# Performance work log

Measured on AMD Instinct MI355X. Metric: run time of the kernel, lower is better.

## Reference

```python
import jax, jax.numpy as jnp
import numpy as np

B, S, D, H = 2, 2048, 1024, 16
HD = D // H  # head dim = 64


def setup_inputs() -> dict:
    key = jax.random.key(0)
    ks = jax.random.split(key, 9)
    s = 1.0 / np.sqrt(D)
    return {
        "hidden_states": jax.random.normal(ks[0], (B, S, D), dtype=jnp.float32),
        "attention_mask": jnp.zeros((B, 1, 1, S), dtype=jnp.float32),
        "Wq": jax.random.normal(ks[1], (D, D), dtype=jnp.float32) * s,
        "bq": jnp.zeros((D,), dtype=jnp.float32),
        "Wk": jax.random.normal(ks[2], (D, D), dtype=jnp.float32) * s,
        "bk": jnp.zeros((D,), dtype=jnp.float32),
        "Wv": jax.random.normal(ks[3], (D, D), dtype=jnp.float32) * s,
        "bv": jnp.zeros((D,), dtype=jnp.float32),
        "Wo": jax.random.normal(ks[4], (D, D), dtype=jnp.float32) * s,
        "bo": jnp.zeros((D,), dtype=jnp.float32),
    }


def reference(hidden_states, attention_mask, Wq, bq, Wk, bk, Wv, bv, Wo, bo):
    b, s = hidden_states.shape[:2]
    # QKV projections -> [b, h, s, hd]
    def proj(W, bias):
        y = hidden_states @ W.T + bias
        return y.reshape(b, s, H, HD).transpose(0, 2, 1, 3)
    q = proj(Wq, bq)
    k = proj(Wk, bk)
    v = proj(Wv, bv)
    scores = jnp.einsum("bhqd,bhkd->bhqk", q, k) / jnp.sqrt(jnp.float32(HD))
    scores = scores + attention_mask  # additive mask, broadcast [b,1,1,s]
    probs = jax.nn.softmax(scores, axis=-1)  # dropout p=0 (eval)
    ctx = jnp.einsum("bhqk,bhkd->bhqd", probs, v)
    ctx = ctx.transpose(0, 2, 1, 3).reshape(b, s, D)
    out = ctx @ Wo.T + bo
    return (out, probs)
```

## Files before the change

kernel.cpp:

```cpp
#include <hip/hip_runtime.h>
#include <hip/hip_bf16.h>

#define B_ 2
#define S_ 2048
#define D_ 1024
#define H_ 16
#define HD_ 64

typedef short bf16x8 __attribute__((ext_vector_type(8)));
typedef float f32x4 __attribute__((ext_vector_type(4)));

typedef __attribute__((address_space(3))) void lds_void;
typedef const __attribute__((address_space(1))) void gbl_void;

__device__ __forceinline__ f32x4 mfma16(bf16x8 a, bf16x8 b, f32x4 c) {
    return __builtin_amdgcn_mfma_f32_16x16x32_bf16(a, b, c, 0, 0, 0);
}

__device__ __forceinline__ bf16x8 ldb8(const __hip_bfloat16* p) {
    return *reinterpret_cast<const bf16x8*>(p);
}

__global__ __launch_bounds__(256) void conv_kernel(const float* __restrict__ src,
                                                   __hip_bfloat16* __restrict__ dst, int n4) {
    int i = blockIdx.x * 256 + threadIdx.x;
    if (i >= n4) return;
    float4 f = reinterpret_cast<const float4*>(src)[i];
    union { __hip_bfloat16 h[4]; ushort4 u; } cv;
    cv.h[0] = __float2bfloat16(f.x);
    cv.h[1] = __float2bfloat16(f.y);
    cv.h[2] = __float2bfloat16(f.z);
    cv.h[3] = __float2bfloat16(f.w);
    reinterpret_cast<ushort4*>(dst)[i] = cv.u;
}

template <int MODE>
__global__ __launch_bounds__(256) void gemm_bt(
    const __hip_bfloat16* __restrict__ X, const __hip_bfloat16* __restrict__ Wt,
    const float* __restrict__ bias0, const float* __restrict__ bias1,
    const float* __restrict__ bias2,
    __hip_bfloat16* __restrict__ Yq, __hip_bfloat16* __restrict__ Yk,
    __hip_bfloat16* __restrict__ Yv, float* __restrict__ Yo,
    int M, int N, int K) {
    __shared__ __hip_bfloat16 As[128 * 32];
    __shared__ __hip_bfloat16 Bs[128 * 32];

    const int ntn = N >> 7;
    const int nwg = (M >> 7) * ntn;
    const int cpx = nwg >> 3;
    const int bid = blockIdx.x;
    const int lg = (bid & 7) * cpx + (bid >> 3);
    const int tm = lg / ntn;
    const int tn = lg % ntn;
    const int t = threadIdx.x;
    const int w = t >> 6, l = t & 63, g = l >> 4, c = l & 15;
    const int wr = w >> 1, wc = w & 1;

    const int lrow16 = l >> 2;
    const int lcol = (l & 3) * 8;

    const int r0 = w * 32 + lrow16;
    const int r1 = w * 32 + 16 + lrow16;
    const size_t xg0 = (size_t)(tm * 128 + r0) * K + lcol;
    const size_t xg1 = (size_t)(tm * 128 + r1) * K + lcol;
    const size_t wg0 = (size_t)(tn * 128 + r0) * K + lcol;
    const size_t wg1 = (size_t)(tn * 128 + r1) * K + lcol;

    f32x4 acc[4][4] = {};

    for (int k0 = 0; k0 < K; k0 += 32) {
        __syncthreads();
        __builtin_amdgcn_global_load_lds((gbl_void*)(X + xg0 + k0),
                                         (lds_void*)(As + (w * 32) * 32), 16, 0, 0);
        __builtin_amdgcn_global_load_lds((gbl_void*)(X + xg1 + k0),
                                         (lds_void*)(As + (w * 32 + 16) * 32), 16, 0, 0);
        __builtin_amdgcn_global_load_lds((gbl_void*)(Wt + wg0 + k0),
                                         (lds_void*)(Bs + (w * 32) * 32), 16, 0, 0);
        __builtin_amdgcn_global_load_lds((gbl_void*)(Wt + wg1 + k0),
                                         (lds_void*)(Bs + (w * 32 + 16) * 32), 16, 0, 0);
        __syncthreads();

        bf16x8 am[4], bn[4];
#pragma unroll
        for (int mi = 0; mi < 4; ++mi) am[mi] = ldb8(&As[(wr * 64 + mi * 16 + c) * 32 + g * 8]);
#pragma unroll
        for (int ni = 0; ni < 4; ++ni) bn[ni] = ldb8(&Bs[(wc * 64 + ni * 16 + c) * 32 + g * 8]);
#pragma unroll
        for (int mi = 0; mi < 4; ++mi)
#pragma unroll
            for (int ni = 0; ni < 4; ++ni)
                acc[mi][ni] = mfma16(am[mi], bn[ni], acc[mi][ni]);
    }

#pragma unroll
    for (int mi = 0; mi < 4; ++mi) {
        const int mbase = tm * 128 + wr * 64 + mi * 16 + g * 4;
#pragma unroll
        for (int ni = 0; ni < 4; ++ni) {
            const int n = tn * 128 + wc * 64 + ni * 16 + c;
#pragma unroll
            for (int r = 0; r < 4; ++r) {
                const int mm = mbase + r;
                float v = acc[mi][ni][r];
                if (MODE == 0) {
                    const float* bp = (n < 1024) ? bias0 : (n < 2048) ? bias1 : bias2;
                    const int nn = n & 1023;
                    v += bp[nn];
                    const int b = mm >> 11, s = mm & 2047;
                    const int h = nn >> 6, hd = nn & 63;
                    const size_t bh = (size_t)(b * H_ + h);
                    const __hip_bfloat16 bvv = __float2bfloat16(v);
                    if (n < 2048) {
                        __hip_bfloat16* dst = (n < 1024) ? Yq : Yk;
                        dst[(bh * S_ + s) * HD_ + hd] = bvv;
                    } else {
                        Yv[(bh * HD_ + hd) * S_ + s] = bvv;
                    }
                } else {
                    Yo[(size_t)mm * N + n] = v + bias0[n];
                }
            }
        }
    }
}

#define STAGE_K(dstc, t8v) do {                                                   \
    const int kt_ = (t8v) * 256;                                                  \
    _Pragma("unroll")                                                             \
    for (int i_ = 0; i_ < 4; ++i_) {                                              \
        const int chunk_ = w * 4 + i_;                                            \
        const int row_ = 8 * chunk_ + (l >> 3);                                   \
        const int col_ = ((l & 7) ^ ((l >> 3) & 7)) * 8;                          \
        __builtin_amdgcn_global_load_lds(                                         \
            (gbl_void*)(Kb + (size_t)(kt_ + row_) * HD_ + col_),                  \
            (lds_void*)((dstc) + chunk_ * 1024), 16, 0, 0);                       \
    }                                                                             \
} while (0)

#define STAGE_V(dstc, t8v) do {                                                   \
    const int kt_ = (t8v) * 256;                                                  \
    _Pragma("unroll")                                                             \
    for (int i_ = 0; i_ < 4; ++i_) {                                              \
        const int chunk_ = w * 4 + i_;                                            \
        const int row_ = 2 * chunk_ + (l >> 5);                                   \
        const int col_ = ((l & 31) ^ (row_ & 7)) * 8;                             \
        __builtin_amdgcn_global_load_lds(                                         \
            (gbl_void*)(Vb + (size_t)row_ * S_ + kt_ + col_),                     \
            (lds_void*)((dstc) + chunk_ * 1024), 16, 0, 0);                       \
    }                                                                             \
} while (0)

__global__ __launch_bounds__(512) void attn_kernel(
    const __hip_bfloat16* __restrict__ Qh, const __hip_bfloat16* __restrict__ Kh,
    const __hip_bfloat16* __restrict__ Vt, const float* __restrict__ mask,
    float* __restrict__ probs, __hip_bfloat16* __restrict__ ctx) {
    union SMem {
        char Kdb[2][32768];
        float Cred[8][16][68];
    };
    __shared__ SMem sm;
    __shared__ float msk[2048];
    __shared__ float sred[8][32];
    __shared__ float invsh[32];

    const int bid = blockIdx.x;
    const int lg = (bid & 7) * 256 + (bid >> 3);
    const int qt = lg & 63;
    const int bh = lg >> 6;
    const int b = bh >> 4, h = bh & 15;
    const int t = threadIdx.x;
    const int w = t >> 6, l = t & 63, g = l >> 4, c = l & 15;
    const int q0 = qt * 32;
    const int kw = 32 * w;

    const __hip_bfloat16* Qb = Qh + (size_t)bh * S_ * HD_;
    const __hip_bfloat16* Kb = Kh + (size_t)bh * S_ * HD_;
    const __hip_bfloat16* Vb = Vt + (size_t)bh * HD_ * S_;
    const float* mrow = mask + (size_t)b * S_;

    *reinterpret_cast<float4*>(&msk[t * 4]) =
        *reinterpret_cast<const float4*>(&mrow[t * 4]);

    const bf16x8 aqA0 = ldb8(&Qb[(q0 + c) * HD_ + g * 8]);
    const bf16x8 aqA1 = ldb8(&Qb[(q0 + c) * HD_ + 32 + g * 8]);
    const bf16x8 aqB0 = ldb8(&Qb[(q0 + 16 + c) * HD_ + g * 8]);
    const bf16x8 aqB1 = ldb8(&Qb[(q0 + 16 + c) * HD_ + 32 + g * 8]);

    unsigned int uA[8][2][2], uB[8][2][2];
    float lsumA = 0.f, lsumB = 0.f;

    STAGE_K(sm.Kdb[0], 0);
#pragma unroll
    for (int t8 = 0; t8 < 8; ++t8) {
        char* cur = sm.Kdb[t8 & 1];
        if (t8 < 7) {
            STAGE_K(sm.Kdb[(t8 & 1) ^ 1], t8 + 1);
            asm volatile("s_waitcnt vmcnt(4)" ::: "memory");
        } else {
            asm volatile("s_waitcnt vmcnt(0)" ::: "memory");
        }
        if (t8 == 0) asm volatile("s_waitcnt lgkmcnt(0)" ::: "memory");
        __builtin_amdgcn_s_barrier();
        __builtin_amdgcn_sched_barrier(0);
        const int kt = t8 * 256;
#pragma unroll
        for (int ss = 0; ss < 2; ++ss) {
            const int krow = kw + ss * 16 + c;
            const char* kb2 = cur + krow * 128;
            const int sw = (krow & 7) << 4;
            const bf16x8 k0 = *reinterpret_cast<const bf16x8*>(kb2 + ((g * 16) ^ sw));
            const bf16x8 k1 = *reinterpret_cast<const bf16x8*>(kb2 + ((64 + g * 16) ^ sw));
            f32x4 aA = {}, aB = {};
            aA = mfma16(k0, aqA0, aA);
            aA = mfma16(k1, aqA1, aA);
            aB = mfma16(k0, aqB0, aB);
            aB = mfma16(k1, aqB1, aB);
            const float4 mk = *reinterpret_cast<const float4*>(&msk[kt + kw + ss * 16 + g * 4]);
            const float pA0 = __expf(aA[0] * 0.125f + mk.x);
            const float pA1 = __expf(aA[1] * 0.125f + mk.y);
            const float pA2 = __expf(aA[2] * 0.125f + mk.z);
            const float pA3 = __expf(aA[3] * 0.125f + mk.w);
            const float pB0 = __expf(aB[0] * 0.125f + mk.x);
            const float pB1 = __expf(aB[1] * 0.125f + mk.y);
            const float pB2 = __expf(aB[2] * 0.125f + mk.z);
            const float pB3 = __expf(aB[3] * 0.125f + mk.w);
            lsumA += (pA0 + pA1) + (pA2 + pA3);
            lsumB += (pB0 + pB1) + (pB2 + pB3);
            union { __hip_bfloat16 hh[2]; unsigned int ui; } w0, w1;
            w0.hh[0] = __float2bfloat16(pA0); w0.hh[1] = __float2bfloat16(pA1);
            w1.hh[0] = __float2bfloat16(pA2); w1.hh[1] = __float2bfloat16(pA3);
            uA[t8][ss][0] = w0.ui; uA[t8][ss][1] = w1.ui;
            w0.hh[0] = __float2bfloat16(pB0); w0.hh[1] = __float2bfloat16(pB1);
            w1.hh[0] = __float2bfloat16(pB2); w1.hh[1] = __float2bfloat16(pB3);
            uB[t8][ss][0] = w0.ui; uB[t8][ss][1] = w1.ui;
        }
        __builtin_amdgcn_sched_barrier(0);
        __builtin_amdgcn_s_barrier();
    }
    lsumA += __shfl_xor(lsumA, 16); lsumA += __shfl_xor(lsumA, 32);
    lsumB += __shfl_xor(lsumB, 16); lsumB += __shfl_xor(lsumB, 32);
    if (g == 0) { sred[w][c] = lsumA; sred[w][16 + c] = lsumB; }
    __syncthreads();
    float totA = 0.f, totB = 0.f;
#pragma unroll
    for (int w8 = 0; w8 < 8; ++w8) { totA += sred[w8][c]; totB += sred[w8][16 + c]; }
    const float invA = 1.0f / totA;
    const float invB = 1.0f / totB;
    if (w == 0 && g == 0) { invsh[c] = invA; invsh[16 + c] = invB; }

    f32x4 caccA[4] = {}, caccB[4] = {};
    float* prowA = probs + ((size_t)bh * S_ + q0 + c) * S_;
    float* prowB = prowA + (size_t)16 * S_;
    const int src0 = 32 * (g & 1) + c;
    const int src1 = src0 + 16;
    const int sigma = g >> 1;
    STAGE_V(sm.Kdb[0], 0);
#pragma unroll
    for (int t8 = 0; t8 < 8; ++t8) {
        char* cur = sm.Kdb[t8 & 1];
        if (t8 < 7) STAGE_V(sm.Kdb[(t8 & 1) ^ 1], t8 + 1);
        if (t8 == 0 || t8 == 7) asm volatile("s_waitcnt vmcnt(4)" ::: "memory");
        else                    asm volatile("s_waitcnt vmcnt(8)" ::: "memory");
        if (t8 == 0) asm volatile("s_waitcnt lgkmcnt(0)" ::: "memory");
        __builtin_amdgcn_s_barrier();
        __builtin_amdgcn_sched_barrier(0);
        const int kt = t8 * 256;
#pragma unroll
        for (int ss = 0; ss < 2; ++ss) {
            f32x4 oA, oB;
            oA[0] = __uint_as_float(uA[t8][ss][0] << 16) * invA;
            oA[1] = __uint_as_float(uA[t8][ss][0] & 0xffff0000u) * invA;
            oA[2] = __uint_as_float(uA[t8][ss][1] << 16) * invA;
            oA[3] = __uint_as_float(uA[t8][ss][1] & 0xffff0000u) * invA;
            *reinterpret_cast<f32x4*>(&prowA[kt + kw + ss * 16 + g * 4]) = oA;
            oB[0] = __uint_as_float(uB[t8][ss][0] << 16) * invB;
            oB[1] = __uint_as_float(uB[t8][ss][0] & 0xffff0000u) * invB;
            oB[2] = __uint_as_float(uB[t8][ss][1] << 16) * invB;
            oB[3] = __uint_as_float(uB[t8][ss][1] & 0xffff0000u) * invB;
            *reinterpret_cast<f32x4*>(&prowB[kt + kw + ss * 16 + g * 4]) = oB;
        }
        union { unsigned int ui[4]; bf16x8 v; } afA, afB;
        {
            const unsigned int x00 = __shfl(uA[t8][0][0], src0);
            const unsigned int x10 = __shfl(uA[t8][1][0], src0);
            const unsigned int x01 = __shfl(uA[t8][0][1], src0);
            const unsigned int x11 = __shfl(uA[t8][1][1], src0);
            const unsigned int x02 = __shfl(uA[t8][0][0], src1);
            const unsigned int x12 = __shfl(uA[t8][1][0], src1);
            const unsigned int x03 = __shfl(uA[t8][0][1], src1);
            const unsigned int x13 = __shfl(uA[t8][1][1], src1);
            afA.ui[0] = sigma ? x10 : x00;
            afA.ui[1] = sigma ? x11 : x01;
            afA.ui[2] = sigma ? x12 : x02;
            afA.ui[3] = sigma ? x13 : x03;
        }
        {
            const unsigned int x00 = __shfl(uB[t8][0][0], src0);
            const unsigned int x10 = __shfl(uB[t8][1][0], src0);
            const unsigned int x01 = __shfl(uB[t8][0][1], src0);
            const unsigned int x11 = __shfl(uB[t8][1][1], src0);
            const unsigned int x02 = __shfl(uB[t8][0][0], src1);
            const unsigned int x12 = __shfl(uB[t8][1][0], src1);
            const unsigned int x03 = __shfl(uB[t8][0][1], src1);
            const unsigned int x13 = __shfl(uB[t8][1][1], src1);
            afB.ui[0] = sigma ? x10 : x00;
            afB.ui[1] = sigma ? x11 : x01;
            afB.ui[2] = sigma ? x12 : x02;
            afB.ui[3] = sigma ? x13 : x03;
        }
#pragma unroll
        for (int n = 0; n < 4; ++n) {
            const int vrow = n * 16 + c;
            const bf16x8 bv = *reinterpret_cast<const bf16x8*>(
                cur + vrow * 512 + ((64 * w + g * 16) ^ ((vrow & 7) << 4)));
            caccA[n] = mfma16(afA.v, bv, caccA[n]);
            caccB[n] = mfma16(afB.v, bv, caccB[n]);
        }
        __builtin_amdgcn_sched_barrier(0);
        __builtin_amdgcn_s_barrier();
    }

    __syncthreads();
#pragma unroll
    for (int n = 0; n < 4; ++n)
#pragma unroll
        for (int r = 0; r < 4; ++r)
            sm.Cred[w][g * 4 + r][n * 16 + c] = caccA[n][r];
    __syncthreads();
    {
        const int row = t >> 5, col2 = (t & 31) * 2;
        float a0 = 0.f, a1 = 0.f;
#pragma unroll
        for (int w8 = 0; w8 < 8; ++w8) {
            const float2 vv = *reinterpret_cast<const float2*>(&sm.Cred[w8][row][col2]);
            a0 += vv.x; a1 += vv.y;
        }
        const float fin = invsh[row];
        union { __hip_bfloat16 hh[2]; unsigned int ui; } ov;
        ov.hh[0] = __float2bfloat16(a0 * fin);
        ov.hh[1] = __float2bfloat16(a1 * fin);
        *reinterpret_cast<unsigned int*>(
            &ctx[((size_t)b * S_ + q0 + row) * D_ + h * HD_ + col2]) = ov.ui;
    }
    __syncthreads();
#pragma unroll
    for (int n = 0; n < 4; ++n)
#pragma unroll
        for (int r = 0; r < 4; ++r)
            sm.Cred[w][g * 4 + r][n * 16 + c] = caccB[n][r];
    __syncthreads();
    {
        const int row = t >> 5, col2 = (t & 31) * 2;
        float a0 = 0.f, a1 = 0.f;
#pragma unroll
        for (int w8 = 0; w8 < 8; ++w8) {
            const float2 vv = *reinterpret_cast<const float2*>(&sm.Cred[w8][row][col2]);
            a0 += vv.x; a1 += vv.y;
        }
        const float fin = invsh[16 + row];
        union { __hip_bfloat16 hh[2]; unsigned int ui; } ov;
        ov.hh[0] = __float2bfloat16(a0 * fin);
        ov.hh[1] = __float2bfloat16(a1 * fin);
        *reinterpret_cast<unsigned int*>(
            &ctx[((size_t)b * S_ + q0 + 16 + row) * D_ + h * HD_ + col2]) = ov.ui;
    }
}

extern "C" void kernel_launch(void* const* d_in, const int* in_sizes, int n_in,
                              void* d_out, int out_size, void* d_ws, size_t ws_size,
                              hipStream_t stream) {
    const float* hs   = (const float*)d_in[0];
    const float* mask = (const float*)d_in[1];
    const float* Wq   = (const float*)d_in[2];
    const float* bq   = (const float*)d_in[3];
    const float* Wk   = (const float*)d_in[4];
    const float* bk   = (const float*)d_in[5];
    const float* Wv   = (const float*)d_in[6];
    const float* bv   = (const float*)d_in[7];
    const float* Wo   = (const float*)d_in[8];
    const float* bo   = (const float*)d_in[9];

    float* out   = (float*)d_out;
    float* probs = out + (size_t)B_ * S_ * D_;

    const size_t MD = (size_t)B_ * S_ * D_;
    __hip_bfloat16* hsb   = (__hip_bfloat16*)d_ws;
    __hip_bfloat16* wqkvb = hsb + MD;
    __hip_bfloat16* wob   = wqkvb + 3u * 1024u * 1024u;
    __hip_bfloat16* Qh    = wob + (size_t)1024 * 1024;
    __hip_bfloat16* Kh    = Qh + MD;
    __hip_bfloat16* Vt    = Kh + MD;
    __hip_bfloat16* ctxb  = Vt + MD;

    conv_kernel<<<4096, 256, 0, stream>>>(hs, hsb, (int)(MD / 4));
    conv_kernel<<<1024, 256, 0, stream>>>(Wq, wqkvb, 262144);
    conv_kernel<<<1024, 256, 0, stream>>>(Wk, wqkvb + 1048576, 262144);
    conv_kernel<<<1024, 256, 0, stream>>>(Wv, wqkvb + 2097152, 262144);
    conv_kernel<<<1024, 256, 0, stream>>>(Wo, wob, 262144);

    gemm_bt<0><<<32 * 24, 256, 0, stream>>>(hsb, wqkvb, bq, bk, bv,
                                            Qh, Kh, Vt, nullptr, 4096, 3072, 1024);

    attn_kernel<<<B_ * H_ * (S_ / 32), 512, 0, stream>>>(Qh, Kh, Vt, mask, probs, ctxb);

    gemm_bt<1><<<32 * 8, 256, 0, stream>>>(ctxb, wob, bo, nullptr, nullptr,
                                           nullptr, nullptr, nullptr, out, 4096, 1024, 1024);
}
```

Before: 325.8 us.

## Halve attention query tile to 16 rows per block for more parallelism

Each attention block now handles 16 query rows instead of 32. This doubles the grid size and roughly halves per-thread register state: one set of probability accumulators and one context accumulator set instead of two. The launch bounds now request 4 blocks per CU, and the vmcnt waits are adjusted for the smaller number of outstanding stores. The cost is that each K/V tile is reloaded twice as often and fewer MFMAs are amortized per LDS read, while LDS use per block may still cap how many blocks fit on a CU.

```diff
diff --git a/kernel.cpp b/kernel.cpp
--- a/kernel.cpp
+++ b/kernel.cpp
@@ -150,7 +150,7 @@
     }                                                                             \
 } while (0)
 
-__global__ __launch_bounds__(512) void attn_kernel(
+__global__ __launch_bounds__(512, 4) void attn_kernel(
     const __hip_bfloat16* __restrict__ Qh, const __hip_bfloat16* __restrict__ Kh,
     const __hip_bfloat16* __restrict__ Vt, const float* __restrict__ mask,
     float* __restrict__ probs, __hip_bfloat16* __restrict__ ctx) {
@@ -160,17 +160,17 @@
     };
     __shared__ SMem sm;
     __shared__ float msk[2048];
-    __shared__ float sred[8][32];
-    __shared__ float invsh[32];
+    __shared__ float sred[8][16];
+    __shared__ float invsh[16];
 
     const int bid = blockIdx.x;
-    const int lg = (bid & 7) * 256 + (bid >> 3);
-    const int qt = lg & 63;
-    const int bh = lg >> 6;
+    const int lg = (bid & 7) * 512 + (bid >> 3);
+    const int qt = lg & 127;
+    const int bh = lg >> 7;
     const int b = bh >> 4, h = bh & 15;
     const int t = threadIdx.x;
     const int w = t >> 6, l = t & 63, g = l >> 4, c = l & 15;
-    const int q0 = qt * 32;
+    const int q0 = qt * 16;
     const int kw = 32 * w;
 
     const __hip_bfloat16* Qb = Qh + (size_t)bh * S_ * HD_;
@@ -181,13 +181,11 @@
     *reinterpret_cast<float4*>(&msk[t * 4]) =
         *reinterpret_cast<const float4*>(&mrow[t * 4]);
 
-    const bf16x8 aqA0 = ldb8(&Qb[(q0 + c) * HD_ + g * 8]);
-    const bf16x8 aqA1 = ldb8(&Qb[(q0 + c) * HD_ + 32 + g * 8]);
-    const bf16x8 aqB0 = ldb8(&Qb[(q0 + 16 + c) * HD_ + g * 8]);
-    const bf16x8 aqB1 = ldb8(&Qb[(q0 + 16 + c) * HD_ + 32 + g * 8]);
-
-    unsigned int uA[8][2][2], uB[8][2][2];
-    float lsumA = 0.f, lsumB = 0.f;
+    const bf16x8 aq0 = ldb8(&Qb[(q0 + c) * HD_ + g * 8]);
+    const bf16x8 aq1 = ldb8(&Qb[(q0 + c) * HD_ + 32 + g * 8]);
+
+    unsigned int uA[8][2][2];
+    float lsum = 0.f;
 
     STAGE_K(sm.Kdb[0], 0);
 #pragma unroll
@@ -210,76 +208,60 @@
             const int sw = (krow & 7) << 4;
             const bf16x8 k0 = *reinterpret_cast<const bf16x8*>(kb2 + ((g * 16) ^ sw));
             const bf16x8 k1 = *reinterpret_cast<const bf16x8*>(kb2 + ((64 + g * 16) ^ sw));
-            f32x4 aA = {}, aB = {};
-            aA = mfma16(k0, aqA0, aA);
-            aA = mfma16(k1, aqA1, aA);
-            aB = mfma16(k0, aqB0, aB);
-            aB = mfma16(k1, aqB1, aB);
+            f32x4 aA = {};
+            aA = mfma16(k0, aq0, aA);
+            aA = mfma16(k1, aq1, aA);
             const float4 mk = *reinterpret_cast<const float4*>(&msk[kt + kw + ss * 16 + g * 4]);
-            const float pA0 = __expf(aA[0] * 0.125f + mk.x);
-            const float pA1 = __expf(aA[1] * 0.125f + mk.y);
-            const float pA2 = __expf(aA[2] * 0.125f + mk.z);
-            const float pA3 = __expf(aA[3] * 0.125f + mk.w);
-            const float pB0 = __expf(aB[0] * 0.125f + mk.x);
-            const float pB1 = __expf(aB[1] * 0.125f + mk.y);
-            const float pB2 = __expf(aB[2] * 0.125f + mk.z);
-            const float pB3 = __expf(aB[3] * 0.125f + mk.w);
-            lsumA += (pA0 + pA1) + (pA2 + pA3);
-            lsumB += (pB0 + pB1) + (pB2 + pB3);
+            const float p0 = __expf(aA[0] * 0.125f + mk.x);
+            const float p1 = __expf(aA[1] * 0.125f + mk.y);
+            const float p2 = __expf(aA[2] * 0.125f + mk.z);
+            const float p3 = __expf(aA[3] * 0.125f + mk.w);
+            lsum += (p0 + p1) + (p2 + p3);
             union { __hip_bfloat16 hh[2]; unsigned int ui; } w0, w1;
-            w0.hh[0] = __float2bfloat16(pA0); w0.hh[1] = __float2bfloat16(pA1);
-            w1.hh[0] = __float2bfloat16(pA2); w1.hh[1] = __float2bfloat16(pA3);
+            w0.hh[0] = __float2bfloat16(p0); w0.hh[1] = __float2bfloat16(p1);
+            w1.hh[0] = __float2bfloat16(p2); w1.hh[1] = __float2bfloat16(p3);
             uA[t8][ss][0] = w0.ui; uA[t8][ss][1] = w1.ui;
-            w0.hh[0] = __float2bfloat16(pB0); w0.hh[1] = __float2bfloat16(pB1);
-            w1.hh[0] = __float2bfloat16(pB2); w1.hh[1] = __float2bfloat16(pB3);
-            uB[t8][ss][0] = w0.ui; uB[t8][ss][1] = w1.ui;
         }
         __builtin_amdgcn_sched_barrier(0);
         __builtin_amdgcn_s_barrier();
     }
-    lsumA += __shfl_xor(lsumA, 16); lsumA += __shfl_xor(lsumA, 32);
-    lsumB += __shfl_xor(lsumB, 16); lsumB += __shfl_xor(lsumB, 32);
-    if (g == 0) { sred[w][c] = lsumA; sred[w][16 + c] = lsumB; }
+
+    lsum += __shfl_xor(lsum, 16);
+    lsum += __shfl_xor(lsum, 32);
+    if (g == 0) sred[w][c] = lsum;
     __syncthreads();
-    float totA = 0.f, totB = 0.f;
-#pragma unroll
-    for (int w8 = 0; w8 < 8; ++w8) { totA += sred[w8][c]; totB += sred[w8][16 + c]; }
-    const float invA = 1.0f / totA;
-    const float invB = 1.0f / totB;
-    if (w == 0 && g == 0) { invsh[c] = invA; invsh[16 + c] = invB; }
-
-    f32x4 caccA[4] = {}, caccB[4] = {};
+    float tot = 0.f;
+#pragma unroll
+    for (int w8 = 0; w8 < 8; ++w8) tot += sred[w8][c];
+    const float invA = 1.0f / tot;
+    if (w == 0 && g == 0) invsh[c] = invA;
+
+    f32x4 cacc[4] = {};
     float* prowA = probs + ((size_t)bh * S_ + q0 + c) * S_;
-    float* prowB = prowA + (size_t)16 * S_;
     const int src0 = 32 * (g & 1) + c;
     const int src1 = src0 + 16;
     const int sigma = g >> 1;
     STAGE_V(sm.Kdb[0], 0);
 #pragma unroll
     for (int t8 = 0; t8 < 8; ++t8) {
-        char* cur = sm.Kdb[t8 & 1];
+        const char* cur = sm.Kdb[t8 & 1];
         if (t8 < 7) STAGE_V(sm.Kdb[(t8 & 1) ^ 1], t8 + 1);
-        if (t8 == 0 || t8 == 7) asm volatile("s_waitcnt vmcnt(4)" ::: "memory");
-        else                    asm volatile("s_waitcnt vmcnt(8)" ::: "memory");
-        if (t8 == 0) asm volatile("s_waitcnt lgkmcnt(0)" ::: "memory");
+        if (t8 == 0)      asm volatile("s_waitcnt vmcnt(4)" ::: "memory");
+        else if (t8 == 7) asm volatile("s_waitcnt vmcnt(2)" ::: "memory");
+        else              asm volatile("s_waitcnt vmcnt(6)" ::: "memory");
         __builtin_amdgcn_s_barrier();
         __builtin_amdgcn_sched_barrier(0);
         const int kt = t8 * 256;
 #pragma unroll
         for (int ss = 0; ss < 2; ++ss) {
-            f32x4 oA, oB;
+            f32x4 oA;
             oA[0] = __uint_as_float(uA[t8][ss][0] << 16) * invA;
             oA[1] = __uint_as_float(uA[t8][ss][0] & 0xffff0000u) * invA;
             oA[2] = __uint_as_float(uA[t8][ss][1] << 16) * invA;
             oA[3] = __uint_as_float(uA[t8][ss][1] & 0xffff0000u) * invA;
             *reinterpret_cast<f32x4*>(&prowA[kt + kw + ss * 16 + g * 4]) = oA;
-            oB[0] = __uint_as_float(uB[t8][ss][0] << 16) * invB;
-            oB[1] = __uint_as_float(uB[t8][ss][0] & 0xffff0000u) * invB;
-            oB[2] = __uint_as_float(uB[t8][ss][1] << 16) * invB;
-            oB[3] = __uint_as_float(uB[t8][ss][1] & 0xffff0000u) * invB;
-            *reinterpret_cast<f32x4*>(&prowB[kt + kw + ss * 16 + g * 4]) = oB;
-        }
-        union { unsigned int ui[4]; bf16x8 v; } afA, afB;
+        }
+        union { unsigned int ui[4]; bf16x8 v; } afA;
         {
             const unsigned int x00 = __shfl(uA[t8][0][0], src0);
             const unsigned int x10 = __shfl(uA[t8][1][0], src0);
@@ -294,27 +276,12 @@
             afA.ui[2] = sigma ? x12 : x02;
             afA.ui[3] = sigma ? x13 : x03;
         }
-        {
-            const unsigned int x00 = __shfl(uB[t8][0][0], src0);
-            const unsigned int x10 = __shfl(uB[t8][1][0], src0);
-            const unsigned int x01 = __shfl(uB[t8][0][1], src0);
-            const unsigned int x11 = __shfl(uB[t8][1][1], src0);
-            const unsigned int x02 = __shfl(uB[t8][0][0], src1);
-            const unsigned int x12 = __shfl(uB[t8][1][0], src1);
-            const unsigned int x03 = __shfl(uB[t8][0][1], src1);
-            const unsigned int x13 = __shfl(uB[t8][1][1], src1);
-            afB.ui[0] = sigma ? x10 : x00;
-            afB.ui[1] = sigma ? x11 : x01;
-            afB.ui[2] = sigma ? x12 : x02;
-            afB.ui[3] = sigma ? x13 : x03;
-        }
 #pragma unroll
         for (int n = 0; n < 4; ++n) {
             const int vrow = n * 16 + c;
             const bf16x8 bv = *reinterpret_cast<const bf16x8*>(
                 cur + vrow * 512 + ((64 * w + g * 16) ^ ((vrow & 7) << 4)));
-            caccA[n] = mfma16(afA.v, bv, caccA[n]);
-            caccB[n] = mfma16(afB.v, bv, caccB[n]);
+            cacc[n] = mfma16(afA.v, bv, cacc[n]);
         }
         __builtin_amdgcn_sched_barrier(0);
         __builtin_amdgcn_s_barrier();
@@ -325,7 +292,7 @@
     for (int n = 0; n < 4; ++n)
 #pragma unroll
         for (int r = 0; r < 4; ++r)
-            sm.Cred[w][g * 4 + r][n * 16 + c] = caccA[n][r];
+            sm.Cred[w][g * 4 + r][n * 16 + c] = cacc[n][r];
     __syncthreads();
     {
         const int row = t >> 5, col2 = (t & 31) * 2;
@@ -341,28 +308,6 @@
         ov.hh[1] = __float2bfloat16(a1 * fin);
         *reinterpret_cast<unsigned int*>(
             &ctx[((size_t)b * S_ + q0 + row) * D_ + h * HD_ + col2]) = ov.ui;
-    }
-    __syncthreads();
-#pragma unroll
-    for (int n = 0; n < 4; ++n)
-#pragma unroll
-        for (int r = 0; r < 4; ++r)
-            sm.Cred[w][g * 4 + r][n * 16 + c] = caccB[n][r];
-    __syncthreads();
-    {
-        const int row = t >> 5, col2 = (t & 31) * 2;
-        float a0 = 0.f, a1 = 0.f;
-#pragma unroll
-        for (int w8 = 0; w8 < 8; ++w8) {
-            const float2 vv = *reinterpret_cast<const float2*>(&sm.Cred[w8][row][col2]);
-            a0 += vv.x; a1 += vv.y;
-        }
-        const float fin = invsh[16 + row];
-        union { __hip_bfloat16 hh[2]; unsigned int ui; } ov;
-        ov.hh[0] = __float2bfloat16(a0 * fin);
-        ov.hh[1] = __float2bfloat16(a1 * fin);
-        *reinterpret_cast<unsigned int*>(
-            &ctx[((size_t)b * S_ + q0 + 16 + row) * D_ + h * HD_ + col2]) = ov.ui;
     }
 }
 
@@ -401,7 +346,7 @@
     gemm_bt<0><<<32 * 24, 256, 0, stream>>>(hsb, wqkvb, bq, bk, bv,
                                             Qh, Kh, Vt, nullptr, 4096, 3072, 1024);
 
-    attn_kernel<<<B_ * H_ * (S_ / 32), 512, 0, stream>>>(Qh, Kh, Vt, mask, probs, ctxb);
+    attn_kernel<<<B_ * H_ * (S_ / 16), 512, 0, stream>>>(Qh, Kh, Vt, mask, probs, ctxb);
 
     gemm_bt<1><<<32 * 8, 256, 0, stream>>>(ctxb, wob, bo, nullptr, nullptr,
                                            nullptr, nullptr, nullptr, out, 4096, 1024, 1024);
```

Measured after the change: 313.7 us. 3.7% less time.
